# Performance work log

Measured on AMD Instinct MI355X. Metric: run time of the kernel, lower is better.

## Reference

```python
import jax, jax.numpy as jnp
import numpy as np

NEG_INF = -9e15


def setup_inputs() -> dict:
    key = jax.random.key(0)
    k1, k2, k3, k4 = jax.random.split(key, 4)
    N, F_in, H, F_out = 4096, 512, 8, 64
    node_features = jax.random.normal(k1, (N, F_in), dtype=jnp.float32)
    adj_matrix = jax.random.randint(k2, (N, N), 0, 2, dtype=jnp.int32)
    # ensure self-loops so every row has at least one unmasked entry
    adj_matrix = jnp.maximum(adj_matrix, jnp.eye(N, dtype=jnp.int32))
    W = jax.random.normal(k3, (H, F_in, F_out), dtype=jnp.float32) * 0.05
    a = jax.random.normal(k4, (H, 2 * F_out), dtype=jnp.float32) * 0.05
    return {"node_features": node_features, "adj_matrix": adj_matrix, "W": W, "a": a}


def reference(node_features, adj_matrix, W, a):
    alpha = 0.2
    H, F_in, F_out = W.shape
    # Per-head linear projection: [H, N, F_out]
    Wh = jnp.einsum("nf,hfo->hno", node_features, W)
    # Attention logits e_ij = LeakyReLU(a1 . Wh_i + a2 . Wh_j)
    f_src = jnp.einsum("hno,ho->hn", Wh, a[:, :F_out])   # [H, N]
    f_dst = jnp.einsum("hno,ho->hn", Wh, a[:, F_out:])   # [H, N]
    e = jax.nn.leaky_relu(f_src[:, :, None] + f_dst[:, None, :], negative_slope=alpha)  # [H, N, N]
    # Mask by adjacency, softmax over neighbors
    masked = jnp.where(adj_matrix[None, :, :] > 0, e, NEG_INF)
    attn = jax.nn.softmax(masked, axis=-1)               # [H, N, N]
    # Aggregate neighbor features per head
    h_prime = jnp.einsum("hnm,hmo->hno", attn, Wh)       # [H, N, F_out]
    # Concat heads along feature dim -> [N, H*F_out]
    return jnp.transpose(h_prime, (1, 0, 2)).reshape(h_prime.shape[1], H * F_out)
```

## Files before the change

### kernel.cpp

```cpp
#include <hip/hip_runtime.h>
#include <stdint.h>


#define NN 4096
#define FIN 512
#define NH 8
#define FO 64

typedef _Float16 f16x8 __attribute__((ext_vector_type(8)));
typedef _Float16 f16x2 __attribute__((ext_vector_type(2)));
typedef __attribute__((ext_vector_type(4))) float f32x4;

union H8 { f16x8 v; f16x2 p[4]; unsigned u[4]; };
union U2 { unsigned u; f16x2 v; };

#define GLOAD_LDS16(g, l)                                                          \
  __builtin_amdgcn_global_load_lds((__attribute__((address_space(1))) const void*)(g), \
                                   (__attribute__((address_space(3))) void*)(l), 16, 0, 0)
#define GLOAD_LDS4(g, l)                                                           \
  __builtin_amdgcn_global_load_lds((__attribute__((address_space(1))) const void*)(g), \
                                   (__attribute__((address_space(3))) void*)(l), 4, 0, 0)

__device__ __forceinline__ unsigned short f2h(float f) {
  _Float16 h = (_Float16)f;
  return __builtin_bit_cast(unsigned short, h);
}

__global__ __launch_bounds__(256) void prep_kernel(
    const float* __restrict__ X, const int* __restrict__ adj, const float* __restrict__ W,
    const float* __restrict__ a,
    unsigned short* __restrict__ Xh, unsigned short* __restrict__ WbT,
    unsigned* __restrict__ adjbitsT, unsigned short* __restrict__ WAh) {
  int bid = blockIdx.x, tid = threadIdx.x;
  if (bid < 2048) {
    int item = bid * 256 + tid;
    int jt = item >> 12, r = item & 4095;
    const int* p = adj + (size_t)r * NN + jt * 32;
    unsigned bits = 0;
#pragma unroll
    for (int b = 0; b < 32; b += 4) {
      int4 v = *(const int4*)(p + b);
      bits |= (unsigned)(v.x & 1) << b;
      bits |= (unsigned)(v.y & 1) << (b + 1);
      bits |= (unsigned)(v.z & 1) << (b + 2);
      bits |= (unsigned)(v.w & 1) << (b + 3);
    }
    adjbitsT[item] = bits;
  } else if (bid < 4096) {
    int item = (bid - 2048) * 256 + tid;
    float4 v = ((const float4*)X)[item];
    ushort4 o;
    o.x = f2h(v.x); o.y = f2h(v.y); o.z = f2h(v.z); o.w = f2h(v.w);
    ((ushort4*)Xh)[item] = o;
  } else if (bid < 5120) {
    int item = (bid - 4096) * 256 + tid;
    int h = item >> 15, rem = item & 32767, o = rem >> 9, k = rem & 511;
    WbT[item] = f2h(W[h * (FIN * FO) + k * FO + o]);
  } else {
    int item = (bid - 5120) * 256 + tid;
    int h = item >> 10, which = (item >> 9) & 1, k = item & 511;
    const float4* wp = (const float4*)(W + ((size_t)h * FIN + k) * FO);
    const float4* ap = (const float4*)(a + h * 128 + which * 64);
    float s = 0.f;
#pragma unroll
    for (int o4 = 0; o4 < 16; ++o4) {
      float4 w4 = wp[o4], a4 = ap[o4];
      s += w4.x * a4.x + w4.y * a4.y + w4.z * a4.z + w4.w * a4.w;
    }
    WAh[(h * 2 + which) * FIN + k] = f2h(s);
  }
}

__global__ __launch_bounds__(512, 4) void proj_sd_kernel(
    const unsigned short* __restrict__ Xh, const unsigned short* __restrict__ WbT,
    const unsigned short* __restrict__ WAh,
    unsigned short* __restrict__ Whfrag, float2* __restrict__ ABf,
    unsigned short* __restrict__ E1h, unsigned short* __restrict__ E2h) {
  __shared__ float red[4 * 64 * 20];
  int lane = threadIdx.x & 63, wave = threadIdx.x >> 6;
  int row16 = lane & 15, grp = lane >> 4;
  int bx = blockIdx.x;
  if (bx >= 512) {
    int i0 = ((bx - 512) * 8 + wave) * 16;
    f32x4 acc = {0, 0, 0, 0};
    const unsigned short* xb = Xh + (size_t)(i0 + row16) * FIN + grp * 8;
    const unsigned short* wb = WAh + row16 * FIN + grp * 8;
#pragma unroll
    for (int k0 = 0; k0 < FIN; k0 += 32)
      acc = __builtin_amdgcn_mfma_f32_16x16x32_f16(*(const f16x8*)(xb + k0),
                                                   *(const f16x8*)(wb + k0), acc, 0, 0, 0);
    int hh = row16 >> 1;
#pragma unroll
    for (int reg = 0; reg < 4; ++reg) {
      int rr = i0 + grp * 4 + reg;
      float v = acc[reg];
      if (row16 & 1) {
        E1h[hh * NN + rr] = f2h(__expf(v));
        E2h[hh * NN + rr] = f2h(__expf(0.2f * v));
      } else {
        ABf[hh * NN + rr] = make_float2(__expf(v), __expf(0.2f * v));
      }
    }
    return;
  }
  int kh = wave >> 2, jb = wave & 3;
  int job = bx * 4 + jb;
  int h = job & 7, rt = job >> 3;
  int i0 = rt * 16;
  f32x4 acc[4] = {{0,0,0,0},{0,0,0,0},{0,0,0,0},{0,0,0,0}};
  const unsigned short* xb = Xh + (size_t)(i0 + row16) * FIN + kh * 256 + grp * 8;
  const unsigned short* wb = WbT + h * (FO * FIN) + row16 * FIN + kh * 256 + grp * 8;
#pragma unroll
  for (int k0 = 0; k0 < 256; k0 += 32) {
    f16x8 af = *(const f16x8*)(xb + k0);
#pragma unroll
    for (int cb = 0; cb < 4; ++cb)
      acc[cb] = __builtin_amdgcn_mfma_f32_16x16x32_f16(
          af, *(const f16x8*)(wb + cb * 16 * FIN + k0), acc[cb], 0, 0, 0);
  }
  if (kh == 1) {
    float* q = red + (jb * 64 + lane) * 20;
#pragma unroll
    for (int cb = 0; cb < 4; ++cb) *(f32x4*)(q + cb * 4) = acc[cb];
  }
  __syncthreads();
  if (kh == 0) {
    const float* q = red + (jb * 64 + lane) * 20;
#pragma unroll
    for (int cb = 0; cb < 4; ++cb) acc[cb] += *(const f32x4*)(q + cb * 4);
    int jt = i0 >> 5;
    int kk0 = (i0 & 31) + grp * 4;
    int tl = (kk0 >> 3) * 16 + row16;
    int e0 = kk0 & 7;
#pragma unroll
    for (int cb = 0; cb < 4; ++cb) {
      ushort4 pk;
      pk.x = f2h(acc[cb][0]); pk.y = f2h(acc[cb][1]);
      pk.z = f2h(acc[cb][2]); pk.w = f2h(acc[cb][3]);
      *(ushort4*)(Whfrag + (((size_t)h * 128 + jt) * 4 + cb) * 512 + tl * 8 + e0) = pk;
    }
  }
}

#define SEGB 4608
#define E_OFF 4096
#define A_OFF 4224

__global__ __launch_bounds__(256, 4) void gat_kernel(
    const unsigned* __restrict__ adjbitsT, const unsigned short* __restrict__ Whfrag,
    const float2* __restrict__ ABf, const unsigned short* __restrict__ E1h,
    const unsigned short* __restrict__ E2h, float* __restrict__ out) {
  __shared__ __align__(16) char lds[8 * SEGB];
  int h = blockIdx.y;
  int lane = threadIdx.x & 63, jseg = threadIdx.x >> 6;
  int row16 = lane & 15, grp = lane >> 4;
  int r0 = blockIdx.x * 32;
  float2 abL = ABf[h * NN + r0 + row16];
  float2 abH = ABf[h * NN + r0 + 16 + row16];
  _Float16 aL = (_Float16)(0.5f * abL.x), bL = (_Float16)(0.5f * abL.y);
  _Float16 aH = (_Float16)(0.5f * abH.x), bH = (_Float16)(0.5f * abH.y);
  f16x2 AhL = {aL, aL}, BhL = {bL, bL}, AhH = {aH, aH}, BhH = {bH, bH};

  H8 ones;
#pragma unroll
  for (int k = 0; k < 4; ++k) ones.u[k] = 0x3C003C00u;

  const unsigned short* wsrc =
      Whfrag + (size_t)h * 262144 + (size_t)jseg * 32 * 2048 + lane * 8;
  const unsigned short* esrc =
      ((lane & 4) ? E2h : E1h) + h * NN + jseg * 1024 + (lane & 3) * 8;
  const unsigned* asrc = adjbitsT + (size_t)(jseg * 32) * NN + r0 + lane;

  f32x4 l0 = {0,0,0,0}, l1 = {0,0,0,0}, l2 = {0,0,0,0}, ld = {0,0,0,0}, lden = {0,0,0,0};
  f32x4 h0 = {0,0,0,0}, h1 = {0,0,0,0}, h2 = {0,0,0,0}, hd = {0,0,0,0}, hden = {0,0,0,0};

  char* seg0 = lds + (jseg * 2 + 0) * SEGB;
  char* seg1 = lds + (jseg * 2 + 1) * SEGB;

  auto stage = [&](char* seg, int p) {
    const unsigned short* bs = wsrc + (size_t)p * 2048;
    GLOAD_LDS16(bs, seg);
    GLOAD_LDS16(bs + 512, seg + 1024);
    GLOAD_LDS16(bs + 1024, seg + 2048);
    GLOAD_LDS16(bs + 1536, seg + 3072);
    if (lane < 32) GLOAD_LDS4(asrc + (size_t)p * NN, seg + A_OFF);
    if (lane < 8)  GLOAD_LDS16(esrc + p * 32, seg + E_OFF);
  };

  auto compute = [&](const char* seg) {
    unsigned bwL = *(const unsigned*)(seg + A_OFF + row16 * 4);
    unsigned bwH = *(const unsigned*)(seg + A_OFF + 64 + row16 * 4);
    unsigned bbL = (bwL >> (grp * 8)) & 0xffu;
    unsigned bbH = (bwH >> (grp * 8)) & 0xffu;
    unsigned tL = bbL | (bbL << 15);
    unsigned tH = bbH | (bbH << 15);
    H8 e1, e2;
    e1.v = *(const f16x8*)(seg + E_OFF + grp * 16);
    e2.v = *(const f16x8*)(seg + E_OFF + 64 + grp * 16);
    const char* bp = seg + lane * 16;
    f16x8 b0 = *(const f16x8*)(bp);
    f16x8 b1 = *(const f16x8*)(bp + 1024);
    f16x8 b2 = *(const f16x8*)(bp + 2048);
    f16x8 b3 = *(const f16x8*)(bp + 3072);
    H8 afL, afH;
#pragma unroll
    for (int k = 0; k < 4; ++k) {
      f16x2 mxL = __builtin_elementwise_max(AhL * e1.p[k], BhL * e2.p[k]);
      f16x2 mxH = __builtin_elementwise_max(AhH * e1.p[k], BhH * e2.p[k]);
      U2 mL, mH;
      mL.u = (tL << (14 - 2 * k)) & 0x40004000u;
      mH.u = (tH << (14 - 2 * k)) & 0x40004000u;
      afL.p[k] = mxL * mL.v;
      afH.p[k] = mxH * mH.v;
    }
    l0   = __builtin_amdgcn_mfma_f32_16x16x32_f16(afL.v, b0, l0, 0, 0, 0);
    l1   = __builtin_amdgcn_mfma_f32_16x16x32_f16(afL.v, b1, l1, 0, 0, 0);
    l2   = __builtin_amdgcn_mfma_f32_16x16x32_f16(afL.v, b2, l2, 0, 0, 0);
    ld   = __builtin_amdgcn_mfma_f32_16x16x32_f16(afL.v, b3, ld, 0, 0, 0);
    lden = __builtin_amdgcn_mfma_f32_16x16x32_f16(afL.v, ones.v, lden, 0, 0, 0);
    h0   = __builtin_amdgcn_mfma_f32_16x16x32_f16(afH.v, b0, h0, 0, 0, 0);
    h1   = __builtin_amdgcn_mfma_f32_16x16x32_f16(afH.v, b1, h1, 0, 0, 0);
    h2   = __builtin_amdgcn_mfma_f32_16x16x32_f16(afH.v, b2, h2, 0, 0, 0);
    hd   = __builtin_amdgcn_mfma_f32_16x16x32_f16(afH.v, b3, hd, 0, 0, 0);
    hden = __builtin_amdgcn_mfma_f32_16x16x32_f16(afH.v, ones.v, hden, 0, 0, 0);
  };

  stage(seg0, 0);
  __syncthreads();
#pragma unroll 1
  for (int p2 = 0; p2 < 16; ++p2) {
    stage(seg1, 2 * p2 + 1);
    compute(seg0);
    __syncthreads();
    if (p2 < 15) stage(seg0, 2 * p2 + 2);
    compute(seg1);
    __syncthreads();
  }

  float* red = (float*)lds;
  if (jseg != 0) {
    float* q = red + ((jseg - 1) * 64 + lane) * 40;
    *(f32x4*)(q +  0) = l0;  *(f32x4*)(q +  4) = l1;
    *(f32x4*)(q +  8) = l2;  *(f32x4*)(q + 12) = ld;
    *(f32x4*)(q + 16) = lden;
    *(f32x4*)(q + 20) = h0;  *(f32x4*)(q + 24) = h1;
    *(f32x4*)(q + 28) = h2;  *(f32x4*)(q + 32) = hd;
    *(f32x4*)(q + 36) = hden;
  }
  __syncthreads();
  if (jseg == 0) {
#pragma unroll
    for (int s = 0; s < 3; ++s) {
      const float* q = red + (s * 64 + lane) * 40;
      l0   += *(const f32x4*)(q +  0);  l1   += *(const f32x4*)(q +  4);
      l2   += *(const f32x4*)(q +  8);  ld   += *(const f32x4*)(q + 12);
      lden += *(const f32x4*)(q + 16);
      h0   += *(const f32x4*)(q + 20);  h1   += *(const f32x4*)(q + 24);
      h2   += *(const f32x4*)(q + 28);  hd   += *(const f32x4*)(q + 32);
      hden += *(const f32x4*)(q + 36);
    }
#pragma unroll
    for (int reg = 0; reg < 4; ++reg) {
      float invL = 1.0f / lden[reg];
      float invH = 1.0f / hden[reg];
      int rowL = r0 + grp * 4 + reg;
      int rowH = r0 + 16 + grp * 4 + reg;
      float* opL = out + (size_t)rowL * (NH * FO) + h * FO + row16;
      float* opH = out + (size_t)rowH * (NH * FO) + h * FO + row16;
      opL[0]  = l0[reg] * invL;  opL[16] = l1[reg] * invL;
      opL[32] = l2[reg] * invL;  opL[48] = ld[reg] * invL;
      opH[0]  = h0[reg] * invH;  opH[16] = h1[reg] * invH;
      opH[32] = h2[reg] * invH;  opH[48] = hd[reg] * invH;
    }
  }
}

extern "C" void kernel_launch(void* const* d_in, const int* in_sizes, int n_in,
                              void* d_out, int out_size, void* d_ws, size_t ws_size,
                              hipStream_t stream) {
  const float* X  = (const float*)d_in[0];
  const int* adj  = (const int*)d_in[1];
  const float* W  = (const float*)d_in[2];
  const float* a  = (const float*)d_in[3];
  float* out = (float*)d_out;
  char* ws = (char*)d_ws;

  unsigned short* Xh     = (unsigned short*)(ws + 0);
  unsigned short* WbT    = (unsigned short*)(ws + 4194304);
  unsigned* adjbitsT     = (unsigned*)(ws + 4718592);
  unsigned short* Whfrag = (unsigned short*)(ws + 6815744);
  unsigned short* WAh    = (unsigned short*)(ws + 11010048);
  float2* ABf            = (float2*)(ws + 11026432);
  unsigned short* E1h    = (unsigned short*)(ws + 11288576);
  unsigned short* E2h    = (unsigned short*)(ws + 11354112);

  prep_kernel<<<5152, 256, 0, stream>>>(X, adj, W, a, Xh, WbT, adjbitsT, WAh);
  proj_sd_kernel<<<544, 512, 0, stream>>>(Xh, WbT, WAh, Whfrag, ABf, E1h, E2h);
  gat_kernel<<<dim3(128, 8), 256, 0, stream>>>(adjbitsT, Whfrag, ABf, E1h, E2h, out);
}
```

Before: 85.57 us.

## Share staged Wh tiles across two row tiles per block and simplify logit math

The GAT kernel now runs 512-thread blocks covering 64 rows, with two row-tile wave groups sharing each staged Wh fragment in LDS. This halves the Wh global traffic per output row. The exp factorisation is reworked to divide the source term out, so each element needs one multiply instead of two inside the max, and the 0.5 scale is folded into the precomputed E arrays. The WbT transpose in prep is rewritten so consecutive threads read W coalesced. In exchange, the kernel needs more LDS and more threads per block, which may cut occupancy. The fp16 range of the per-row ratio exp(-0.8 v) is also a risk.

```diff
diff --git a/kernel.cpp b/kernel.cpp
--- a/kernel.cpp
+++ b/kernel.cpp
@@ -54,8 +54,8 @@
     ((ushort4*)Xh)[item] = o;
   } else if (bid < 5120) {
     int item = (bid - 4096) * 256 + tid;
-    int h = item >> 15, rem = item & 32767, o = rem >> 9, k = rem & 511;
-    WbT[item] = f2h(W[h * (FIN * FO) + k * FO + o]);
+    int o = item & 63, k = (item >> 6) & 511, h = item >> 15;
+    WbT[h * 32768 + o * 512 + k] = f2h(W[h * 32768 + k * 64 + o]);
   } else {
     int item = (bid - 5120) * 256 + tid;
     int h = item >> 10, which = (item >> 9) & 1, k = item & 511;
@@ -74,7 +74,7 @@
 __global__ __launch_bounds__(512, 4) void proj_sd_kernel(
     const unsigned short* __restrict__ Xh, const unsigned short* __restrict__ WbT,
     const unsigned short* __restrict__ WAh,
-    unsigned short* __restrict__ Whfrag, float2* __restrict__ ABf,
+    unsigned short* __restrict__ Whfrag, float* __restrict__ Rf,
     unsigned short* __restrict__ E1h, unsigned short* __restrict__ E2h) {
   __shared__ float red[4 * 64 * 20];
   int lane = threadIdx.x & 63, wave = threadIdx.x >> 6;
@@ -82,6 +82,7 @@
   int bx = blockIdx.x;
   if (bx >= 512) {
     int i0 = ((bx - 512) * 8 + wave) * 16;
+    if (i0 >= NN) return;
     f32x4 acc = {0, 0, 0, 0};
     const unsigned short* xb = Xh + (size_t)(i0 + row16) * FIN + grp * 8;
     const unsigned short* wb = WAh + row16 * FIN + grp * 8;
@@ -95,10 +96,10 @@
       int rr = i0 + grp * 4 + reg;
       float v = acc[reg];
       if (row16 & 1) {
-        E1h[hh * NN + rr] = f2h(__expf(v));
-        E2h[hh * NN + rr] = f2h(__expf(0.2f * v));
+        E1h[hh * NN + rr] = f2h(0.5f * __expf(v));
+        E2h[hh * NN + rr] = f2h(0.5f * __expf(0.2f * v));
       } else {
-        ABf[hh * NN + rr] = make_float2(__expf(v), __expf(0.2f * v));
+        Rf[hh * NN + rr] = __expf(-0.8f * v);
       }
     }
     return;
@@ -146,20 +147,21 @@
 #define E_OFF 4096
 #define A_OFF 4224
 
-__global__ __launch_bounds__(256, 4) void gat_kernel(
+__global__ __launch_bounds__(512, 4) void gat_kernel(
     const unsigned* __restrict__ adjbitsT, const unsigned short* __restrict__ Whfrag,
-    const float2* __restrict__ ABf, const unsigned short* __restrict__ E1h,
+    const float* __restrict__ Rf, const unsigned short* __restrict__ E1h,
     const unsigned short* __restrict__ E2h, float* __restrict__ out) {
-  __shared__ __align__(16) char lds[8 * SEGB];
+  __shared__ __align__(16) char lds[61440];
   int h = blockIdx.y;
-  int lane = threadIdx.x & 63, jseg = threadIdx.x >> 6;
+  int lane = threadIdx.x & 63, wave = threadIdx.x >> 6;
   int row16 = lane & 15, grp = lane >> 4;
-  int r0 = blockIdx.x * 32;
-  float2 abL = ABf[h * NN + r0 + row16];
-  float2 abH = ABf[h * NN + r0 + 16 + row16];
-  _Float16 aL = (_Float16)(0.5f * abL.x), bL = (_Float16)(0.5f * abL.y);
-  _Float16 aH = (_Float16)(0.5f * abH.x), bH = (_Float16)(0.5f * abH.y);
-  f16x2 AhL = {aL, aL}, BhL = {bL, bL}, AhH = {aH, aH}, BhH = {bH, bH};
+  int rt = wave >> 2, jseg = wave & 3;
+  int r0 = blockIdx.x * 64;
+  int rbase = r0 + rt * 32;
+  float RL = Rf[h * NN + rbase + row16];
+  float RH = Rf[h * NN + rbase + 16 + row16];
+  _Float16 rl = (_Float16)RL, rh = (_Float16)RH;
+  f16x2 RhL = {rl, rl}, RhH = {rh, rh};
 
   H8 ones;
 #pragma unroll
@@ -178,18 +180,21 @@
   char* seg1 = lds + (jseg * 2 + 1) * SEGB;
 
   auto stage = [&](char* seg, int p) {
-    const unsigned short* bs = wsrc + (size_t)p * 2048;
-    GLOAD_LDS16(bs, seg);
-    GLOAD_LDS16(bs + 512, seg + 1024);
-    GLOAD_LDS16(bs + 1024, seg + 2048);
-    GLOAD_LDS16(bs + 1536, seg + 3072);
-    if (lane < 32) GLOAD_LDS4(asrc + (size_t)p * NN, seg + A_OFF);
-    if (lane < 8)  GLOAD_LDS16(esrc + p * 32, seg + E_OFF);
+    if (rt == 0) {
+      const unsigned short* bs = wsrc + (size_t)p * 2048;
+      GLOAD_LDS16(bs, seg);
+      GLOAD_LDS16(bs + 512, seg + 1024);
+      GLOAD_LDS16(bs + 1024, seg + 2048);
+      GLOAD_LDS16(bs + 1536, seg + 3072);
+    } else {
+      GLOAD_LDS4(asrc + (size_t)p * NN, seg + A_OFF);
+      if (lane < 8) GLOAD_LDS16(esrc + p * 32, seg + E_OFF);
+    }
   };
 
   auto compute = [&](const char* seg) {
-    unsigned bwL = *(const unsigned*)(seg + A_OFF + row16 * 4);
-    unsigned bwH = *(const unsigned*)(seg + A_OFF + 64 + row16 * 4);
+    unsigned bwL = *(const unsigned*)(seg + A_OFF + (rt * 32 + row16) * 4);
+    unsigned bwH = *(const unsigned*)(seg + A_OFF + (rt * 32 + 16 + row16) * 4);
     unsigned bbL = (bwL >> (grp * 8)) & 0xffu;
     unsigned bbH = (bwH >> (grp * 8)) & 0xffu;
     unsigned tL = bbL | (bbL << 15);
@@ -205,8 +210,8 @@
     H8 afL, afH;
 #pragma unroll
     for (int k = 0; k < 4; ++k) {
-      f16x2 mxL = __builtin_elementwise_max(AhL * e1.p[k], BhL * e2.p[k]);
-      f16x2 mxH = __builtin_elementwise_max(AhH * e1.p[k], BhH * e2.p[k]);
+      f16x2 mxL = __builtin_elementwise_max(e1.p[k], RhL * e2.p[k]);
+      f16x2 mxH = __builtin_elementwise_max(e1.p[k], RhH * e2.p[k]);
       U2 mL, mH;
       mL.u = (tL << (14 - 2 * k)) & 0x40004000u;
       mH.u = (tH << (14 - 2 * k)) & 0x40004000u;
@@ -239,7 +244,7 @@
 
   float* red = (float*)lds;
   if (jseg != 0) {
-    float* q = red + ((jseg - 1) * 64 + lane) * 40;
+    float* q = red + (((jseg - 1) * 2 + rt) * 64 + lane) * 40;
     *(f32x4*)(q +  0) = l0;  *(f32x4*)(q +  4) = l1;
     *(f32x4*)(q +  8) = l2;  *(f32x4*)(q + 12) = ld;
     *(f32x4*)(q + 16) = lden;
@@ -251,7 +256,7 @@
   if (jseg == 0) {
 #pragma unroll
     for (int s = 0; s < 3; ++s) {
-      const float* q = red + (s * 64 + lane) * 40;
+      const float* q = red + ((s * 2 + rt) * 64 + lane) * 40;
       l0   += *(const f32x4*)(q +  0);  l1   += *(const f32x4*)(q +  4);
       l2   += *(const f32x4*)(q +  8);  ld   += *(const f32x4*)(q + 12);
       lden += *(const f32x4*)(q + 16);
@@ -263,8 +268,8 @@
     for (int reg = 0; reg < 4; ++reg) {
       float invL = 1.0f / lden[reg];
       float invH = 1.0f / hden[reg];
-      int rowL = r0 + grp * 4 + reg;
-      int rowH = r0 + 16 + grp * 4 + reg;
+      int rowL = rbase + grp * 4 + reg;
+      int rowH = rbase + 16 + grp * 4 + reg;
       float* opL = out + (size_t)rowL * (NH * FO) + h * FO + row16;
       float* opH = out + (size_t)rowH * (NH * FO) + h * FO + row16;
       opL[0]  = l0[reg] * invL;  opL[16] = l1[reg] * invL;
@@ -290,11 +295,11 @@
   unsigned* adjbitsT     = (unsigned*)(ws + 4718592);
   unsigned short* Whfrag = (unsigned short*)(ws + 6815744);
   unsigned short* WAh    = (unsigned short*)(ws + 11010048);
-  float2* ABf            = (float2*)(ws + 11026432);
+  float* Rf              = (float*)(ws + 11026432);
   unsigned short* E1h    = (unsigned short*)(ws + 11288576);
   unsigned short* E2h    = (unsigned short*)(ws + 11354112);
 
   prep_kernel<<<5152, 256, 0, stream>>>(X, adj, W, a, Xh, WbT, adjbitsT, WAh);
-  proj_sd_kernel<<<544, 512, 0, stream>>>(Xh, WbT, WAh, Whfrag, ABf, E1h, E2h);
-  gat_kernel<<<dim3(128, 8), 256, 0, stream>>>(adjbitsT, Whfrag, ABf, E1h, E2h, out);
-}
+  proj_sd_kernel<<<544, 512, 0, stream>>>(Xh, WbT, WAh, Whfrag, Rf, E1h, E2h);
+  gat_kernel<<<dim3(64, 8), 512, 0, stream>>>(adjbitsT, Whfrag, Rf, E1h, E2h, out);
+}
```

Result: faster. 79.77 us (-6.8%).
